# Optimization experiments

Hardware: AMD Instinct MI355X
Metric: run time of the kernel (lower is better)

## Reference

```python
import jax, jax.numpy as jnp
import numpy as np
from jax import lax

B, L, D, H = 32, 2048, 1024, 16
CHUNK, MEM = 128, 64
PROB, SKILL = 1200, 234
T = MEM + CHUNK
HD = D // H
EPS = 1e-5

# static block mask: mem tokens fully visible, causal within chunk part
_mask_np = np.zeros((T, T), dtype=bool)
_mask_np[MEM:, MEM:] = np.triu(np.ones((CHUNK, CHUNK), dtype=bool), k=1)
MASK = jnp.asarray(_mask_np)


def _ln(x, g, b):
    mu = jnp.mean(x, axis=-1, keepdims=True)
    var = jnp.mean((x - mu) ** 2, axis=-1, keepdims=True)
    return (x - mu) * lax.rsqrt(var + EPS) * g + b


def setup_inputs() -> dict:
    key = jax.random.key(0)
    ks = jax.random.split(key, 12)
    nrm = lambda k, shape: jax.random.normal(k, shape, jnp.float32) * 0.02
    emb_prob = nrm(ks[0], (PROB, D)).at[0].set(0.0)   # padding_idx=0
    emb_skill = nrm(ks[1], (SKILL, D)).at[0].set(0.0)
    return {
        "in_prob": jax.random.randint(ks[9], (B, L), 0, PROB, dtype=jnp.int32),
        "in_skill": jax.random.randint(ks[10], (B, L), 0, SKILL, dtype=jnp.int32),
        "emb_prob": emb_prob,
        "emb_skill": emb_skill,
        "mem_init": nrm(ks[2], (1, MEM, D)),
        "pos_emb": nrm(ks[3], (T, D)),
        "wqkv": nrm(ks[4], (3 * D, D)), "bqkv": jnp.zeros(3 * D, jnp.float32),
        "wo": nrm(ks[5], (D, D)), "bo": jnp.zeros(D, jnp.float32),
        "w1": nrm(ks[6], (4 * D, D)), "b1": jnp.zeros(4 * D, jnp.float32),
        "w2": nrm(ks[7], (D, 4 * D)), "b2": jnp.zeros(D, jnp.float32),
        "ln_a_g": jnp.ones(D, jnp.float32), "ln_a_b": jnp.zeros(D, jnp.float32),
        "ln_f_g": jnp.ones(D, jnp.float32), "ln_f_b": jnp.zeros(D, jnp.float32),
        "gw": nrm(ks[8], (D, D)), "gb": jnp.zeros(D, jnp.float32),
    }


def reference(in_prob, in_skill, emb_prob, emb_skill, mem_init, pos_emb,
              wqkv, bqkv, wo, bo, w1, b1, w2, b2,
              ln_a_g, ln_a_b, ln_f_g, ln_f_b, gw, gb):
    x = emb_prob[in_prob] + emb_skill[in_skill]          # [B,L,D]
    nC = L // CHUNK
    xs = x.reshape(B, nC, CHUNK, D).transpose(1, 0, 2, 3)  # [nC,B,CHUNK,D]
    mem0 = jnp.broadcast_to(mem_init, (B, MEM, D))

    def mha(z):  # z: [B,T,D]
        qkv = z @ wqkv.T + bqkv                          # [B,T,3D]
        q, k, v = jnp.split(qkv, 3, axis=-1)
        q = q.reshape(B, T, H, HD).transpose(0, 2, 1, 3)
        k = k.reshape(B, T, H, HD).transpose(0, 2, 1, 3)
        v = v.reshape(B, T, H, HD).transpose(0, 2, 1, 3)
        scores = jnp.einsum("bhqd,bhkd->bhqk", q, k) / jnp.sqrt(jnp.float32(HD))
        scores = jnp.where(MASK, -jnp.inf, scores)
        attn = jax.nn.softmax(scores, axis=-1)
        o = jnp.einsum("bhqk,bhkd->bhqd", attn, v)
        o = o.transpose(0, 2, 1, 3).reshape(B, T, D)
        return o @ wo.T + bo

    def step(mem, inp):
        chunk, idx = inp
        z = jnp.concatenate([mem, chunk], axis=1) + pos_emb[None]  # [B,T,D]
        z = z + mha(_ln(z, ln_a_g, ln_a_b))
        zf = _ln(z, ln_f_g, ln_f_b)
        z = z + (jax.nn.relu(zf @ w1.T + b1) @ w2.T + b2)
        h = z[:, MEM:, :]
        cand = z[:, :MEM, :]
        g = jax.nn.sigmoid(cand @ gw.T + gb)
        mem_new = jnp.where(idx == 0, cand, g * cand + (1.0 - g) * mem)
        return mem_new, h

    mem_fin, hs = lax.scan(step, mem0, (xs, jnp.arange(nC)))
    out = hs.transpose(1, 0, 2, 3).reshape(B, L, D)
    return out, mem_fin
```

## Files before the change

### kernel.cpp

```cpp
#include <hip/hip_runtime.h>
#include <cstdint>

typedef __attribute__((ext_vector_type(4))) float f32x4;
typedef __attribute__((ext_vector_type(8))) short s16x8;
typedef __attribute__((ext_vector_type(8))) unsigned short u16x8;
typedef __attribute__((ext_vector_type(4))) unsigned short u16x4;

#define DEVI __device__ __forceinline__

namespace {

constexpr int B = 32, L = 2048, D = 1024, H = 16;
constexpr int CHUNK = 128, MEM = 64, T = 192;
constexpr int NC = 16;

DEVI unsigned short f2bf(float f) {
  unsigned x = __builtin_bit_cast(unsigned, f);
  return (unsigned short)((x + 0x7fffu + ((x >> 16) & 1u)) >> 16);
}

typedef const __attribute__((address_space(1))) unsigned char ga_t;
typedef __attribute__((address_space(3))) unsigned char la_t;

DEVI void gload16(const void* g, void* l) {
  __builtin_amdgcn_global_load_lds((ga_t*)g, (la_t*)l, 16, 0, 0);
}

__global__ void k_cvt(const float* __restrict__ in, unsigned short* __restrict__ out, int n) {
  int i = blockIdx.x * 256 + threadIdx.x;
  if (i < n) out[i] = f2bf(in[i]);
}

__global__ void k_copy_mem(const float* __restrict__ src, float* __restrict__ dst) {
  int i = blockIdx.x * 256 + threadIdx.x;
  dst[i] = src[i];
}

template<int MODE>
__global__ __launch_bounds__(256) void k_lnw(
    const float* __restrict__ memb, const float* __restrict__ mem_init,
    const float* __restrict__ pos,
    const float* __restrict__ embP, const float* __restrict__ embS,
    const int* __restrict__ ipr, const int* __restrict__ isk,
    const float* __restrict__ gg, const float* __restrict__ bb,
    float* __restrict__ z, unsigned short* __restrict__ lnout,
    const float* __restrict__ pp, const float* __restrict__ bo, int t)
{
  const int tid = threadIdx.x, lane = tid & 63, wid = tid >> 6;
  const int row = blockIdx.x * 4 + wid;
  const int b = row / T, i = row % T;
  const int c0 = lane * 4;

  float v[16];
  if constexpr (MODE == 0) {
    if (i < MEM) {
      const float* src = (t == 0) ? (mem_init + (size_t)i * D)
                                  : (memb + ((size_t)b * MEM + i) * D);
      #pragma unroll
      for (int k = 0; k < 4; ++k) {
        const int c = k * 256 + c0;
        const f32x4 s = *reinterpret_cast<const f32x4*>(&src[c]);
        const f32x4 p = *reinterpret_cast<const f32x4*>(&pos[i * D + c]);
        #pragma unroll
        for (int e = 0; e < 4; ++e) v[k * 4 + e] = s[e] + p[e];
      }
    } else {
      const int j = t * CHUNK + (i - MEM);
      const int pi = ipr[b * L + j], si = isk[b * L + j];
      #pragma unroll
      for (int k = 0; k < 4; ++k) {
        const int c = k * 256 + c0;
        const f32x4 ep = *reinterpret_cast<const f32x4*>(&embP[(size_t)pi * D + c]);
        const f32x4 es = *reinterpret_cast<const f32x4*>(&embS[(size_t)si * D + c]);
        const f32x4 p  = *reinterpret_cast<const f32x4*>(&pos[i * D + c]);
        #pragma unroll
        for (int e = 0; e < 4; ++e) v[k * 4 + e] = ep[e] + es[e] + p[e];
      }
    }
  } else {
    const size_t MN = (size_t)B * T * D;
    #pragma unroll
    for (int k = 0; k < 4; ++k) {
      const int c = k * 256 + c0;
      const f32x4 zz = *reinterpret_cast<const f32x4*>(&z[(size_t)row * D + c]);
      const f32x4 p0 = *reinterpret_cast<const f32x4*>(&pp[(size_t)row * D + c]);
      const f32x4 p1 = *reinterpret_cast<const f32x4*>(&pp[MN + (size_t)row * D + c]);
      const f32x4 bv = *reinterpret_cast<const f32x4*>(&bo[c]);
      #pragma unroll
      for (int e = 0; e < 4; ++e) v[k * 4 + e] = zz[e] + p0[e] + p1[e] + bv[e];
    }
  }
  float s = 0.f, s2 = 0.f;
  #pragma unroll
  for (int e = 0; e < 16; ++e) { s += v[e]; s2 += v[e] * v[e]; }
  #pragma unroll
  for (int m = 1; m < 64; m <<= 1) { s += __shfl_xor(s, m, 64); s2 += __shfl_xor(s2, m, 64); }
  const float mu  = s * (1.0f / 1024.0f);
  const float var = s2 * (1.0f / 1024.0f) - mu * mu;
  const float rs  = rsqrtf(var + 1e-5f);
  #pragma unroll
  for (int k = 0; k < 4; ++k) {
    f32x4 zz = {v[k*4+0], v[k*4+1], v[k*4+2], v[k*4+3]};
    *reinterpret_cast<f32x4*>(&z[(size_t)row * D + k * 256 + c0]) = zz;
  }
  #pragma unroll
  for (int k = 0; k < 4; ++k) {
    const int c = k * 256 + c0;
    u16x4 o;
    #pragma unroll
    for (int e = 0; e < 4; ++e)
      o[e] = f2bf((v[k * 4 + e] - mu) * rs * gg[c + e] + bb[c + e]);
    *reinterpret_cast<u16x4*>(&lnout[(size_t)row * D + c]) = o;
  }
}

struct GArgs {
  const unsigned short* A; const unsigned short* W; const float* bias;
  unsigned short* outb; float* z; float* outf; unsigned short* candb; float* mem;
  int M, N, K, t;
};

template<int EPI, int SPLITK>
__global__ __launch_bounds__(256) void k_gemmp(GArgs a)
{
  __shared__ __align__(16) unsigned short Al[2][128 * 32];
  __shared__ __align__(16) unsigned short Bl[2][128 * 32];
  const int tid = threadIdx.x;
  const int lane = tid & 63, wid = tid >> 6;
  const int gx = gridDim.x;
  const int nwg = gx * gridDim.y;
  const int f = blockIdx.y * gx + blockIdx.x;
  const int tile = (f & 7) * (nwg >> 3) + (f >> 3);
  const int brow = (tile / gx) * 128, bcol = (tile % gx) * 128;
  const int wr = wid >> 1, wc = wid & 1;
  const int c0 = lane & 15, g4 = lane >> 4;
  const int K = a.K;
  const int Ks = K / SPLITK;
  const int kbase = blockIdx.z * Ks;

  const int r0 = tid >> 2, oc8 = (tid & 3) * 8;
  const int dst0 = wid * 512, dst1 = 2048 + wid * 512;

  f32x4 acc[4][4] = {};

  const unsigned short* __restrict__ Ag = a.A;
  const unsigned short* __restrict__ Wg = a.W;

  auto stage = [&](int t1, int buf) {
    const int kb = kbase + t1 * 32;
    gload16(&Ag[(size_t)(brow + r0) * K + kb + oc8],      &Al[buf][dst0]);
    gload16(&Ag[(size_t)(brow + 64 + r0) * K + kb + oc8], &Al[buf][dst1]);
    gload16(&Wg[(size_t)(bcol + r0) * K + kb + oc8],      &Bl[buf][dst0]);
    gload16(&Wg[(size_t)(bcol + 64 + r0) * K + kb + oc8], &Bl[buf][dst1]);
  };

  stage(0, 0);
  const int nt = Ks >> 5;
  int cur = 0;
  for (int t = 0; t < nt; ++t) {
    __syncthreads();
    if (t + 1 < nt) stage(t + 1, cur ^ 1);
    s16x8 af[4], bf[4];
    #pragma unroll
    for (int m = 0; m < 4; ++m)
      af[m] = *reinterpret_cast<const s16x8*>(&Al[cur][(wr * 64 + m * 16 + c0) * 32 + g4 * 8]);
    #pragma unroll
    for (int n = 0; n < 4; ++n)
      bf[n] = *reinterpret_cast<const s16x8*>(&Bl[cur][(wc * 64 + n * 16 + c0) * 32 + g4 * 8]);
    #pragma unroll
    for (int m = 0; m < 4; ++m)
      #pragma unroll
      for (int n = 0; n < 4; ++n)
        acc[m][n] = __builtin_amdgcn_mfma_f32_16x16x32_bf16(af[m], bf[n], acc[m][n], 0, 0, 0);
    cur ^= 1;
  }

  #pragma unroll
  for (int m = 0; m < 4; ++m) {
    #pragma unroll
    for (int n = 0; n < 4; ++n) {
      const int col = bcol + wc * 64 + n * 16 + c0;
      float bv = 0.f;
      if constexpr (EPI != 8) bv = a.bias[col];
      #pragma unroll
      for (int j = 0; j < 4; ++j) {
        const int row = brow + wr * 64 + m * 16 + g4 * 4 + j;
        float v = acc[m][n][j] + bv;
        if constexpr (EPI == 0) {
          a.outb[(size_t)row * a.N + col] = f2bf(v);
        } else if constexpr (EPI == 1) {
          a.outb[(size_t)row * a.N + col] = f2bf(v > 0.f ? v : 0.f);
        } else if constexpr (EPI == 8) {
          a.outf[(size_t)blockIdx.z * a.M * a.N + (size_t)row * a.N + col] = v;
        }
      }
    }
  }
}

__global__ __launch_bounds__(256) void k_red2(
    const float* __restrict__ p, float* __restrict__ z, const float* __restrict__ bias,
    float* __restrict__ out, unsigned short* __restrict__ candb, int t)
{
  const int row = blockIdx.x;
  const int b = row / T, i = row % T;
  const int c = threadIdx.x * 4;
  const size_t MN = (size_t)B * T * D;
  const f32x4 p0 = *reinterpret_cast<const f32x4*>(&p[(size_t)row * D + c]);
  const f32x4 p1 = *reinterpret_cast<const f32x4*>(&p[MN + (size_t)row * D + c]);
  const f32x4 bb = *reinterpret_cast<const f32x4*>(&bias[c]);
  const f32x4 zz = *reinterpret_cast<const f32x4*>(&z[(size_t)row * D + c]);
  f32x4 zv;
  #pragma unroll
  for (int e = 0; e < 4; ++e) zv[e] = zz[e] + p0[e] + p1[e] + bb[e];
  if (i < MEM) {
    *reinterpret_cast<f32x4*>(&z[(size_t)row * D + c]) = zv;
    u16x4 o;
    #pragma unroll
    for (int e = 0; e < 4; ++e) o[e] = f2bf(zv[e]);
    *reinterpret_cast<u16x4*>(&candb[((size_t)b * MEM + i) * D + c]) = o;
  } else {
    *reinterpret_cast<f32x4*>(&out[((size_t)b * L + t * CHUNK + (i - MEM)) * D + c]) = zv;
  }
}

__global__ __launch_bounds__(256) void k_redg(
    const float* __restrict__ p, const float* __restrict__ z,
    const float* __restrict__ gb, float* __restrict__ memb, int t)
{
  const int row = blockIdx.x;
  const int b = row >> 6, i = row & 63;
  const int c = threadIdx.x * 4;
  const size_t MN = (size_t)B * MEM * D;
  f32x4 s = *reinterpret_cast<const f32x4*>(&gb[c]);
  #pragma unroll
  for (int k = 0; k < 4; ++k) {
    const f32x4 pk = *reinterpret_cast<const f32x4*>(&p[k * MN + (size_t)row * D + c]);
    #pragma unroll
    for (int e = 0; e < 4; ++e) s[e] += pk[e];
  }
  const f32x4 cand = *reinterpret_cast<const f32x4*>(&z[((size_t)b * T + i) * D + c]);
  f32x4 mo = *reinterpret_cast<f32x4*>(&memb[(size_t)row * D + c]);
  f32x4 r;
  #pragma unroll
  for (int e = 0; e < 4; ++e) {
    const float g = 1.0f / (1.0f + __expf(-s[e]));
    r[e] = (t == 0) ? cand[e] : g * cand[e] + (1.0f - g) * mo[e];
  }
  *reinterpret_cast<f32x4*>(&memb[(size_t)row * D + c]) = r;
}

__global__ __launch_bounds__(256) void k_attn(const unsigned short* __restrict__ qkv,
                                              unsigned short* __restrict__ attno)
{
  __shared__ unsigned short Ks[192 * 64];
  __shared__ unsigned short Vt[64 * 192];
  __shared__ unsigned short Pl[4][16 * 200];
  const int tid = threadIdx.x, lane = tid & 63, wid = tid >> 6;
  const int b = blockIdx.x >> 4, h = blockIdx.x & 15;
  const size_t base = (size_t)b * T * 3072 + h * 64;

  #pragma unroll
  for (int it = 0; it < 6; ++it) {
    const int cidx = tid + it * 256;
    const int key = cidx >> 3, hb = cidx & 7;
    const u16x8 kv = *reinterpret_cast<const u16x8*>(&qkv[base + (size_t)key * 3072 + 1024 + hb * 8]);
    *reinterpret_cast<u16x8*>(&Ks[key * 64 + ((hb ^ (key & 7)) * 8)]) = kv;
    const u16x8 vv = *reinterpret_cast<const u16x8*>(&qkv[base + (size_t)key * 3072 + 2048 + hb * 8]);
    #pragma unroll
    for (int e = 0; e < 8; ++e) {
      const int hd = hb * 8 + e;
      Vt[hd * 192 + (((key >> 3) + hd) % 24) * 8 + (key & 7)] = vv[e];
    }
  }
  __syncthreads();

  const int c0 = lane & 15, g4 = lane >> 4;
  for (int qb = wid; qb < 12; qb += 4) {
    s16x8 qf[2];
    #pragma unroll
    for (int kk = 0; kk < 2; ++kk)
      qf[kk] = *reinterpret_cast<const s16x8*>(&qkv[base + (size_t)(qb * 16 + c0) * 3072 + kk * 32 + g4 * 8]);
    f32x4 sc[12];
    #pragma unroll
    for (int cb = 0; cb < 12; ++cb) {
      f32x4 s4 = {};
      #pragma unroll
      for (int kk = 0; kk < 2; ++kk) {
        const s16x8 kf = *reinterpret_cast<const s16x8*>(
            &Ks[(cb * 16 + c0) * 64 + (((kk * 4 + g4) ^ (c0 & 7)) * 8)]);
        s4 = __builtin_amdgcn_mfma_f32_16x16x32_bf16(qf[kk], kf, s4, 0, 0, 0);
      }
      sc[cb] = s4;
    }
    #pragma unroll
    for (int j = 0; j < 4; ++j) {
      const int qi = qb * 16 + g4 * 4 + j;
      float mj = -1e30f;
      #pragma unroll
      for (int cb = 0; cb < 12; ++cb) {
        const int kj = cb * 16 + c0;
        float sv = sc[cb][j] * 0.125f;
        if (qi >= MEM && kj > qi) sv = -1e30f;
        sc[cb][j] = sv;
        mj = fmaxf(mj, sv);
      }
      #pragma unroll
      for (int msk = 1; msk <= 8; msk <<= 1) mj = fmaxf(mj, __shfl_xor(mj, msk, 64));
      float sum = 0.f;
      #pragma unroll
      for (int cb = 0; cb < 12; ++cb) {
        const float p = exp2f((sc[cb][j] - mj) * 1.44269504f);
        sc[cb][j] = p;
        sum += p;
      }
      #pragma unroll
      for (int msk = 1; msk <= 8; msk <<= 1) sum += __shfl_xor(sum, msk, 64);
      const float rin = 1.0f / sum;
      #pragma unroll
      for (int cb = 0; cb < 12; ++cb)
        Pl[wid][(g4 * 4 + j) * 200 + cb * 16 + c0] = f2bf(sc[cb][j] * rin);
    }
    #pragma unroll
    for (int cb2 = 0; cb2 < 4; ++cb2) {
      f32x4 ao = {};
      const int hd = cb2 * 16 + c0;
      #pragma unroll
      for (int kk = 0; kk < 6; ++kk) {
        const int k0 = kk * 32 + g4 * 8;
        const s16x8 pf = *reinterpret_cast<const s16x8*>(&Pl[wid][c0 * 200 + k0]);
        const s16x8 vf = *reinterpret_cast<const s16x8*>(&Vt[hd * 192 + (((k0 >> 3) + hd) % 24) * 8]);
        ao = __builtin_amdgcn_mfma_f32_16x16x32_bf16(pf, vf, ao, 0, 0, 0);
      }
      #pragma unroll
      for (int j = 0; j < 4; ++j) {
        const int q = qb * 16 + g4 * 4 + j;
        attno[((size_t)b * T + q) * D + h * 64 + cb2 * 16 + c0] = f2bf(ao[j]);
      }
    }
  }
}

}

extern "C" void kernel_launch(void* const* d_in, const int* in_sizes, int n_in,
                              void* d_out, int out_size, void* d_ws, size_t ws_size,
                              hipStream_t stream)
{
  const int*   ipr      = (const int*)d_in[0];
  const int*   isk      = (const int*)d_in[1];
  const float* embP     = (const float*)d_in[2];
  const float* embS     = (const float*)d_in[3];
  const float* mem_init = (const float*)d_in[4];
  const float* pos      = (const float*)d_in[5];
  const float* wqkv     = (const float*)d_in[6];
  const float* bqkv     = (const float*)d_in[7];
  const float* wo       = (const float*)d_in[8];
  const float* bo       = (const float*)d_in[9];
  const float* w1       = (const float*)d_in[10];
  const float* b1       = (const float*)d_in[11];
  const float* w2       = (const float*)d_in[12];
  const float* b2       = (const float*)d_in[13];
  const float* ln_a_g   = (const float*)d_in[14];
  const float* ln_a_b   = (const float*)d_in[15];
  const float* ln_f_g   = (const float*)d_in[16];
  const float* ln_f_b   = (const float*)d_in[17];
  const float* gw       = (const float*)d_in[18];
  const float* gb       = (const float*)d_in[19];
  float* out = (float*)d_out;
  (void)in_sizes; (void)n_in; (void)out_size; (void)ws_size;

  char* ws = (char*)d_ws;
  size_t off = 0;
  auto alloc = [&](size_t bytes) -> void* {
    void* p = ws + off; off += (bytes + 255) & ~(size_t)255; return p;
  };
  unsigned short* wqkv_b = (unsigned short*)alloc((size_t)3072 * 1024 * 2);
  unsigned short* wo_b   = (unsigned short*)alloc((size_t)1024 * 1024 * 2);
  unsigned short* w1_b   = (unsigned short*)alloc((size_t)4096 * 1024 * 2);
  unsigned short* w2_b   = (unsigned short*)alloc((size_t)1024 * 4096 * 2);
  unsigned short* gw_b   = (unsigned short*)alloc((size_t)1024 * 1024 * 2);
  float*          z      = (float*)alloc((size_t)B * T * D * 4);
  unsigned short* lnb    = (unsigned short*)alloc((size_t)B * T * D * 2);
  unsigned short* atno   = (unsigned short*)alloc((size_t)B * T * D * 2);
  unsigned short* big    = (unsigned short*)alloc((size_t)B * T * 4096 * 2);
  unsigned short* candb  = (unsigned short*)alloc((size_t)B * MEM * D * 2);
  float*          memb   = (float*)alloc((size_t)B * MEM * D * 4);
  float*          p2     = (float*)alloc((size_t)2 * B * T * D * 4);
  float*          p4     = (float*)alloc((size_t)4 * B * MEM * D * 4);

  k_cvt<<<(3072 * 1024) / 256, 256, 0, stream>>>(wqkv, wqkv_b, 3072 * 1024);
  k_cvt<<<(1024 * 1024) / 256, 256, 0, stream>>>(wo,   wo_b,   1024 * 1024);
  k_cvt<<<(4096 * 1024) / 256, 256, 0, stream>>>(w1,   w1_b,   4096 * 1024);
  k_cvt<<<(1024 * 4096) / 256, 256, 0, stream>>>(w2,   w2_b,   1024 * 4096);
  k_cvt<<<(1024 * 1024) / 256, 256, 0, stream>>>(gw,   gw_b,   1024 * 1024);

  for (int t = 0; t < NC; ++t) {
    k_lnw<0><<<(B * T) / 4, 256, 0, stream>>>(memb, mem_init, pos, embP, embS, ipr, isk,
                                              ln_a_g, ln_a_b, z, lnb, nullptr, nullptr, t);
    { GArgs a{lnb, wqkv_b, bqkv, big, nullptr, nullptr, nullptr, nullptr, B * T, 3072, 1024, t};
      k_gemmp<0, 1><<<dim3(3072 / 128, (B * T) / 128), 256, 0, stream>>>(a); }
    k_attn<<<B * H, 256, 0, stream>>>(big, atno);
    { GArgs a{atno, wo_b, nullptr, nullptr, nullptr, p2, nullptr, nullptr, B * T, 1024, 1024, t};
      k_gemmp<8, 2><<<dim3(1024 / 128, (B * T) / 128, 2), 256, 0, stream>>>(a); }
    k_lnw<2><<<(B * T) / 4, 256, 0, stream>>>(nullptr, nullptr, nullptr, nullptr, nullptr,
                                              nullptr, nullptr, ln_f_g, ln_f_b, z, lnb,
                                              p2, bo, t);
    { GArgs a{lnb, w1_b, b1, big, nullptr, nullptr, nullptr, nullptr, B * T, 4096, 1024, t};
      k_gemmp<1, 1><<<dim3(4096 / 128, (B * T) / 128), 256, 0, stream>>>(a); }
    { GArgs a{big, w2_b, nullptr, nullptr, nullptr, p2, nullptr, nullptr, B * T, 1024, 4096, t};
      k_gemmp<8, 2><<<dim3(1024 / 128, (B * T) / 128, 2), 256, 0, stream>>>(a); }
    k_red2<<<B * T, 256, 0, stream>>>(p2, z, b2, out, candb, t);
    { GArgs a{candb, gw_b, nullptr, nullptr, nullptr, p4, nullptr, nullptr, B * MEM, 1024, 1024, t};
      k_gemmp<8, 4><<<dim3(1024 / 128, (B * MEM) / 128, 4), 256, 0, stream>>>(a); }
    k_redg<<<B * MEM, 256, 0, stream>>>(p4, z, gb, memb, t);
  }
  k_copy_mem<<<(B * MEM * D) / 256, 256, 0, stream>>>(memb, out + (size_t)B * L * D);
}
```

Before: 4.756 ms.

## Store split-K partials in bf16 and fuse gate update into next LayerNorm

Split-K GEMM partial outputs (p2, p4) are now written and read as bf16 instead of fp32, which halves that partial-sum traffic. The gate reduction and memory update is fused with the next step's LayerNorm over the memory rows, and a separate kernel handles the chunk rows, replacing the full k_lnw<0> pass for t>0. Attention MFMA sections are also wrapped with s_setprio. Rounding partial sums to bf16 before the reduction adds numerical error to the residual stream.

Result: faster. 4.449 ms (-6.5%).

```diff
diff --git a/kernel.cpp b/kernel.cpp
--- a/kernel.cpp
+++ b/kernel.cpp
@@ -17,6 +17,9 @@
 DEVI unsigned short f2bf(float f) {
   unsigned x = __builtin_bit_cast(unsigned, f);
   return (unsigned short)((x + 0x7fffu + ((x >> 16) & 1u)) >> 16);
+}
+DEVI float bf2f(unsigned short u) {
+  return __builtin_bit_cast(float, (unsigned)u << 16);
 }
 
 typedef const __attribute__((address_space(1))) unsigned char ga_t;
@@ -44,7 +47,7 @@
     const int* __restrict__ ipr, const int* __restrict__ isk,
     const float* __restrict__ gg, const float* __restrict__ bb,
     float* __restrict__ z, unsigned short* __restrict__ lnout,
-    const float* __restrict__ pp, const float* __restrict__ bo, int t)
+    const unsigned short* __restrict__ pp, const float* __restrict__ bo, int t)
 {
   const int tid = threadIdx.x, lane = tid & 63, wid = tid >> 6;
   const int row = blockIdx.x * 4 + wid;
@@ -83,11 +86,12 @@
     for (int k = 0; k < 4; ++k) {
       const int c = k * 256 + c0;
       const f32x4 zz = *reinterpret_cast<const f32x4*>(&z[(size_t)row * D + c]);
-      const f32x4 p0 = *reinterpret_cast<const f32x4*>(&pp[(size_t)row * D + c]);
-      const f32x4 p1 = *reinterpret_cast<const f32x4*>(&pp[MN + (size_t)row * D + c]);
+      const u16x4 p0 = *reinterpret_cast<const u16x4*>(&pp[(size_t)row * D + c]);
+      const u16x4 p1 = *reinterpret_cast<const u16x4*>(&pp[MN + (size_t)row * D + c]);
       const f32x4 bv = *reinterpret_cast<const f32x4*>(&bo[c]);
       #pragma unroll
-      for (int e = 0; e < 4; ++e) v[k * 4 + e] = zz[e] + p0[e] + p1[e] + bv[e];
+      for (int e = 0; e < 4; ++e)
+        v[k * 4 + e] = zz[e] + bf2f(p0[e]) + bf2f(p1[e]) + bv[e];
     }
   }
   float s = 0.f, s2 = 0.f;
@@ -112,6 +116,108 @@
       o[e] = f2bf((v[k * 4 + e] - mu) * rs * gg[c + e] + bb[c + e]);
     *reinterpret_cast<u16x4*>(&lnout[(size_t)row * D + c]) = o;
   }
+}
+
+__global__ __launch_bounds__(256) void k_ln0c(
+    const float* __restrict__ pos,
+    const float* __restrict__ embP, const float* __restrict__ embS,
+    const int* __restrict__ ipr, const int* __restrict__ isk,
+    const float* __restrict__ gg, const float* __restrict__ bb,
+    float* __restrict__ z, unsigned short* __restrict__ lnout, int t)
+{
+  const int tid = threadIdx.x, lane = tid & 63, wid = tid >> 6;
+  const int q = blockIdx.x * 4 + wid;
+  const int b = q >> 7, j = q & 127;
+  const int i = MEM + j;
+  const int row = b * T + i;
+  const int c0 = lane * 4;
+  const int pi = ipr[b * L + t * CHUNK + j], si = isk[b * L + t * CHUNK + j];
+
+  float v[16];
+  #pragma unroll
+  for (int k = 0; k < 4; ++k) {
+    const int c = k * 256 + c0;
+    const f32x4 ep = *reinterpret_cast<const f32x4*>(&embP[(size_t)pi * D + c]);
+    const f32x4 es = *reinterpret_cast<const f32x4*>(&embS[(size_t)si * D + c]);
+    const f32x4 p  = *reinterpret_cast<const f32x4*>(&pos[i * D + c]);
+    #pragma unroll
+    for (int e = 0; e < 4; ++e) v[k * 4 + e] = ep[e] + es[e] + p[e];
+  }
+  float s = 0.f, s2 = 0.f;
+  #pragma unroll
+  for (int e = 0; e < 16; ++e) { s += v[e]; s2 += v[e] * v[e]; }
+  #pragma unroll
+  for (int m = 1; m < 64; m <<= 1) { s += __shfl_xor(s, m, 64); s2 += __shfl_xor(s2, m, 64); }
+  const float mu  = s * (1.0f / 1024.0f);
+  const float var = s2 * (1.0f / 1024.0f) - mu * mu;
+  const float rs  = rsqrtf(var + 1e-5f);
+  #pragma unroll
+  for (int k = 0; k < 4; ++k) {
+    f32x4 zz = {v[k*4+0], v[k*4+1], v[k*4+2], v[k*4+3]};
+    *reinterpret_cast<f32x4*>(&z[(size_t)row * D + k * 256 + c0]) = zz;
+  }
+  #pragma unroll
+  for (int k = 0; k < 4; ++k) {
+    const int c = k * 256 + c0;
+    u16x4 o;
+    #pragma unroll
+    for (int e = 0; e < 4; ++e)
+      o[e] = f2bf((v[k * 4 + e] - mu) * rs * gg[c + e] + bb[c + e]);
+    *reinterpret_cast<u16x4*>(&lnout[(size_t)row * D + c]) = o;
+  }
+}
+
+__global__ __launch_bounds__(256) void k_redg_ln(
+    const unsigned short* __restrict__ p, float* __restrict__ z,
+    const float* __restrict__ gb, float* __restrict__ memb, int tprev,
+    const float* __restrict__ pos, const float* __restrict__ gg,
+    const float* __restrict__ bb, unsigned short* __restrict__ lnout)
+{
+  const int row = blockIdx.x;
+  const int b = row >> 6, i = row & 63;
+  const int tid = threadIdx.x;
+  const int c = tid * 4;
+  const size_t MN = (size_t)B * MEM * D;
+  const size_t zi = ((size_t)b * T + i) * D + c;
+
+  f32x4 sacc = *reinterpret_cast<const f32x4*>(&gb[c]);
+  #pragma unroll
+  for (int k = 0; k < 4; ++k) {
+    const u16x4 pk = *reinterpret_cast<const u16x4*>(&p[k * MN + (size_t)row * D + c]);
+    #pragma unroll
+    for (int e = 0; e < 4; ++e) sacc[e] += bf2f(pk[e]);
+  }
+  const f32x4 cand = *reinterpret_cast<const f32x4*>(&z[zi]);
+  const f32x4 mo   = *reinterpret_cast<const f32x4*>(&memb[(size_t)row * D + c]);
+  const f32x4 pp4  = *reinterpret_cast<const f32x4*>(&pos[i * D + c]);
+  f32x4 r, v;
+  #pragma unroll
+  for (int e = 0; e < 4; ++e) {
+    const float g = 1.0f / (1.0f + __expf(-sacc[e]));
+    r[e] = (tprev == 0) ? cand[e] : g * cand[e] + (1.0f - g) * mo[e];
+    v[e] = r[e] + pp4[e];
+  }
+  *reinterpret_cast<f32x4*>(&memb[(size_t)row * D + c]) = r;
+
+  float s = v[0] + v[1] + v[2] + v[3];
+  float s2 = v[0]*v[0] + v[1]*v[1] + v[2]*v[2] + v[3]*v[3];
+  #pragma unroll
+  for (int m = 1; m < 64; m <<= 1) { s += __shfl_xor(s, m, 64); s2 += __shfl_xor(s2, m, 64); }
+  __shared__ float ps[4], ps2[4];
+  const int wid = tid >> 6;
+  if ((tid & 63) == 0) { ps[wid] = s; ps2[wid] = s2; }
+  __syncthreads();
+  s  = ps[0] + ps[1] + ps[2] + ps[3];
+  s2 = ps2[0] + ps2[1] + ps2[2] + ps2[3];
+  const float mu  = s * (1.0f / 1024.0f);
+  const float var = s2 * (1.0f / 1024.0f) - mu * mu;
+  const float rs  = rsqrtf(var + 1e-5f);
+  *reinterpret_cast<f32x4*>(&z[zi]) = v;
+  u16x4 o;
+  #pragma unroll
+  for (int e = 0; e < 4; ++e)
+    o[e] = f2bf((v[e] - mu) * rs * gg[c + e] + bb[c + e]);
+  *reinterpret_cast<u16x4*>(&lnout[zi]) = o;
 }
 
 struct GArgs {
@@ -181,7 +287,7 @@
     for (int n = 0; n < 4; ++n) {
       const int col = bcol + wc * 64 + n * 16 + c0;
       float bv = 0.f;
-      if constexpr (EPI != 8) bv = a.bias[col];
+      if constexpr (EPI != 9) bv = a.bias[col];
       #pragma unroll
       for (int j = 0; j < 4; ++j) {
         const int row = brow + wr * 64 + m * 16 + g4 * 4 + j;
@@ -190,8 +296,8 @@
           a.outb[(size_t)row * a.N + col] = f2bf(v);
         } else if constexpr (EPI == 1) {
           a.outb[(size_t)row * a.N + col] = f2bf(v > 0.f ? v : 0.f);
-        } else if constexpr (EPI == 8) {
-          a.outf[(size_t)blockIdx.z * a.M * a.N + (size_t)row * a.N + col] = v;
+        } else if constexpr (EPI == 9) {
+          a.outb[(size_t)blockIdx.z * a.M * a.N + (size_t)row * a.N + col] = f2bf(v);
         }
       }
     }
@@ -199,20 +305,21 @@
 }
 
 __global__ __launch_bounds__(256) void k_red2(
-    const float* __restrict__ p, float* __restrict__ z, const float* __restrict__ bias,
+    const unsigned short* __restrict__ p, float* __restrict__ z,
+    const float* __restrict__ bias,
     float* __restrict__ out, unsigned short* __restrict__ candb, int t)
 {
   const int row = blockIdx.x;
   const int b = row / T, i = row % T;
   const int c = threadIdx.x * 4;
   const size_t MN = (size_t)B * T * D;
-  const f32x4 p0 = *reinterpret_cast<const f32x4*>(&p[(size_t)row * D + c]);
-  const f32x4 p1 = *reinterpret_cast<const f32x4*>(&p[MN + (size_t)row * D + c]);
+  const u16x4 p0 = *reinterpret_cast<const u16x4*>(&p[(size_t)row * D + c]);
+  const u16x4 p1 = *reinterpret_cast<const u16x4*>(&p[MN + (size_t)row * D + c]);
   const f32x4 bb = *reinterpret_cast<const f32x4*>(&bias[c]);
   const f32x4 zz = *reinterpret_cast<const f32x4*>(&z[(size_t)row * D + c]);
   f32x4 zv;
   #pragma unroll
-  for (int e = 0; e < 4; ++e) zv[e] = zz[e] + p0[e] + p1[e] + bb[e];
+  for (int e = 0; e < 4; ++e) zv[e] = zz[e] + bf2f(p0[e]) + bf2f(p1[e]) + bb[e];
   if (i < MEM) {
     *reinterpret_cast<f32x4*>(&z[(size_t)row * D + c]) = zv;
     u16x4 o;
@@ -225,7 +332,7 @@
 }
 
 __global__ __launch_bounds__(256) void k_redg(
-    const float* __restrict__ p, const float* __restrict__ z,
+    const unsigned short* __restrict__ p, const float* __restrict__ z,
     const float* __restrict__ gb, float* __restrict__ memb, int t)
 {
   const int row = blockIdx.x;
@@ -235,9 +342,9 @@
   f32x4 s = *reinterpret_cast<const f32x4*>(&gb[c]);
   #pragma unroll
   for (int k = 0; k < 4; ++k) {
-    const f32x4 pk = *reinterpret_cast<const f32x4*>(&p[k * MN + (size_t)row * D + c]);
-    #pragma unroll
-    for (int e = 0; e < 4; ++e) s[e] += pk[e];
+    const u16x4 pk = *reinterpret_cast<const u16x4*>(&p[k * MN + (size_t)row * D + c]);
+    #pragma unroll
+    for (int e = 0; e < 4; ++e) s[e] += bf2f(pk[e]);
   }
   const f32x4 cand = *reinterpret_cast<const f32x4*>(&z[((size_t)b * T + i) * D + c]);
   f32x4 mo = *reinterpret_cast<f32x4*>(&memb[(size_t)row * D + c]);
@@ -282,6 +389,7 @@
     for (int kk = 0; kk < 2; ++kk)
       qf[kk] = *reinterpret_cast<const s16x8*>(&qkv[base + (size_t)(qb * 16 + c0) * 3072 + kk * 32 + g4 * 8]);
     f32x4 sc[12];
+    __builtin_amdgcn_s_setprio(1);
     #pragma unroll
     for (int cb = 0; cb < 12; ++cb) {
       f32x4 s4 = {};
@@ -293,6 +401,7 @@
       }
       sc[cb] = s4;
     }
+    __builtin_amdgcn_s_setprio(0);
     #pragma unroll
     for (int j = 0; j < 4; ++j) {
       const int qi = qb * 16 + g4 * 4 + j;
@@ -325,6 +434,7 @@
     for (int cb2 = 0; cb2 < 4; ++cb2) {
       f32x4 ao = {};
       const int hd = cb2 * 16 + c0;
+      __builtin_amdgcn_s_setprio(1);
       #pragma unroll
       for (int kk = 0; kk < 6; ++kk) {
         const int k0 = kk * 32 + g4 * 8;
@@ -332,6 +442,7 @@
         const s16x8 vf = *reinterpret_cast<const s16x8*>(&Vt[hd * 192 + (((k0 >> 3) + hd) % 24) * 8]);
         ao = __builtin_amdgcn_mfma_f32_16x16x32_bf16(pf, vf, ao, 0, 0, 0);
       }
+      __builtin_amdgcn_s_setprio(0);
       #pragma unroll
       for (int j = 0; j < 4; ++j) {
         const int q = qb * 16 + g4 * 4 + j;
@@ -386,8 +497,8 @@
   unsigned short* big    = (unsigned short*)alloc((size_t)B * T * 4096 * 2);
   unsigned short* candb  = (unsigned short*)alloc((size_t)B * MEM * D * 2);
   float*          memb   = (float*)alloc((size_t)B * MEM * D * 4);
-  float*          p2     = (float*)alloc((size_t)2 * B * T * D * 4);
-  float*          p4     = (float*)alloc((size_t)4 * B * MEM * D * 4);
+  unsigned short* p2     = (unsigned short*)alloc((size_t)2 * B * T * D * 2);
+  unsigned short* p4     = (unsigned short*)alloc((size_t)4 * B * MEM * D * 2);
 
   k_cvt<<<(3072 * 1024) / 256, 256, 0, stream>>>(wqkv, wqkv_b, 3072 * 1024);
   k_cvt<<<(1024 * 1024) / 256, 256, 0, stream>>>(wo,   wo_b,   1024 * 1024);
@@ -396,24 +507,31 @@
   k_cvt<<<(1024 * 1024) / 256, 256, 0, stream>>>(gw,   gw_b,   1024 * 1024);
 
   for (int t = 0; t < NC; ++t) {
-    k_lnw<0><<<(B * T) / 4, 256, 0, stream>>>(memb, mem_init, pos, embP, embS, ipr, isk,
-                                              ln_a_g, ln_a_b, z, lnb, nullptr, nullptr, t);
+    if (t == 0) {
+      k_lnw<0><<<(B * T) / 4, 256, 0, stream>>>(memb, mem_init, pos, embP, embS, ipr, isk,
+                                                ln_a_g, ln_a_b, z, lnb, nullptr, nullptr, t);
+    } else {
+      k_redg_ln<<<B * MEM, 256, 0, stream>>>(p4, z, gb, memb, t - 1,
+                                             pos, ln_a_g, ln_a_b, lnb);
+      k_ln0c<<<(B * CHUNK) / 4, 256, 0, stream>>>(pos, embP, embS, ipr, isk,
+                                                  ln_a_g, ln_a_b, z, lnb, t);
+    }
     { GArgs a{lnb, wqkv_b, bqkv, big, nullptr, nullptr, nullptr, nullptr, B * T, 3072, 1024, t};
       k_gemmp<0, 1><<<dim3(3072 / 128, (B * T) / 128), 256, 0, stream>>>(a); }
     k_attn<<<B * H, 256, 0, stream>>>(big, atno);
-    { GArgs a{atno, wo_b, nullptr, nullptr, nullptr, p2, nullptr, nullptr, B * T, 1024, 1024, t};
-      k_gemmp<8, 2><<<dim3(1024 / 128, (B * T) / 128, 2), 256, 0, stream>>>(a); }
+    { GArgs a{atno, wo_b, nullptr, p2, nullptr, nullptr, nullptr, nullptr, B * T, 1024, 1024, t};
+      k_gemmp<9, 2><<<dim3(1024 / 128, (B * T) / 128, 2), 256, 0, stream>>>(a); }
     k_lnw<2><<<(B * T) / 4, 256, 0, stream>>>(nullptr, nullptr, nullptr, nullptr, nullptr,
                                               nullptr, nullptr, ln_f_g, ln_f_b, z, lnb,
                                               p2, bo, t);
     { GArgs a{lnb, w1_b, b1, big, nullptr, nullptr, nullptr, nullptr, B * T, 4096, 1024, t};
       k_gemmp<1, 1><<<dim3(4096 / 128, (B * T) / 128), 256, 0, stream>>>(a); }
-    { GArgs a{big, w2_b, nullptr, nullptr, nullptr, p2, nullptr, nullptr, B * T, 1024, 4096, t};
-      k_gemmp<8, 2><<<dim3(1024 / 128, (B * T) / 128, 2), 256, 0, stream>>>(a); }
+    { GArgs a{big, w2_b, nullptr, p2, nullptr, nullptr, nullptr, nullptr, B * T, 1024, 4096, t};
+      k_gemmp<9, 2><<<dim3(1024 / 128, (B * T) / 128, 2), 256, 0, stream>>>(a); }
     k_red2<<<B * T, 256, 0, stream>>>(p2, z, b2, out, candb, t);
-    { GArgs a{candb, gw_b, nullptr, nullptr, nullptr, p4, nullptr, nullptr, B * MEM, 1024, 1024, t};
-      k_gemmp<8, 4><<<dim3(1024 / 128, (B * MEM) / 128, 4), 256, 0, stream>>>(a); }
-    k_redg<<<B * MEM, 256, 0, stream>>>(p4, z, gb, memb, t);
-  }
+    { GArgs a{candb, gw_b, nullptr, p4, nullptr, nullptr, nullptr, nullptr, B * MEM, 1024, 1024, t};
+      k_gemmp<9, 4><<<dim3(1024 / 128, (B * MEM) / 128, 4), 256, 0, stream>>>(a); }
+  }
+  k_redg<<<B * MEM, 256, 0, stream>>>(p4, z, gb, memb, NC - 1);
   k_copy_mem<<<(B * MEM * D) / 256, 256, 0, stream>>>(memb, out + (size_t)B * L * D);
 }
```
